# Kernel optimization log

Measured on AMD Instinct MI355X. Metric: run time of the kernel, lower is better.

The kernel has to match this reference:

```python
import jax, jax.numpy as jnp
import numpy as np

TOP_K = 2
NEG_INF = -1e30


def setup_inputs() -> dict:
    key = jax.random.key(0)
    ks = jax.random.split(key, 9)
    S, B, D, H, E, O = 2, 2048, 1024, 2048, 8, 1024
    return {
        "xs": jax.random.normal(ks[0], (S, B, D), jnp.float32),
        "Wg": jax.random.normal(ks[1], (D, E), jnp.float32),
        "b": jax.random.normal(ks[2], (E,), jnp.float32),
        "fc1_w": jax.random.normal(ks[3], (E, H, D), jnp.float32) * 0.02,
        "fc1_b": jax.random.normal(ks[4], (E, H), jnp.float32) * 0.02,
        "fc2_w": jax.random.normal(ks[5], (E, H, H), jnp.float32) * 0.02,
        "fc2_b": jax.random.normal(ks[6], (E, H), jnp.float32) * 0.02,
        "final_w": jax.random.normal(ks[7], (O, H), jnp.float32) * 0.02,
        "final_b": jax.random.normal(ks[8], (O,), jnp.float32) * 0.02,
    }


def reference(xs, Wg, b, fc1_w, fc1_b, fc2_w, fc2_b, final_w, final_b):
    # xs: [S, B, D] stacked x_list
    S = xs.shape[0]
    # gate logits H: [S, B, E]
    Hg = jnp.einsum('sbd,de->sbe', xs, Wg) + b
    expert_probs = jax.nn.softmax(Hg, axis=-1)  # per-view full softmax
    # top-k threshold mask (H >= kth largest value)
    topk_vals = jax.lax.top_k(Hg, TOP_K)[0]          # [S, B, K]
    thr = topk_vals[..., -1:]                         # [S, B, 1]
    H_masked = jnp.where(Hg >= thr, Hg, NEG_INF)
    G = jax.nn.softmax(H_masked, axis=-1)             # [S, B, E]
    # dense all-expert FFN: [S, B, E, H]
    h = jnp.einsum('sbd,ehd->sbeh', xs, fc1_w) + fc1_b
    h = jax.nn.relu(h)
    eo = jnp.einsum('sbeh,egh->sbeg', h, fc2_w) + fc2_b
    # gated sum over experts, averaged over views: [B, H]
    combined = jnp.einsum('sbe,sbeh->bh', G, eo) / S
    out = combined @ final_w.T + final_b               # [B, O]
    return out, expert_probs
```

## Files before the change

### kernel.cpp

```cpp
#include <hip/hip_runtime.h>
#include <stdint.h>

#define S_DIM 2
#define B_DIM 2048
#define D_DIM 1024
#define H_DIM 2048
#define E_DIM 8
#define O_DIM 1024
#define NTOK 4096
#define CAP 12288

typedef __attribute__((ext_vector_type(8))) short bf16x8;
typedef __attribute__((ext_vector_type(4))) float f32x4;

__device__ __forceinline__ unsigned short f2bf(float f) {
    union { float f; uint32_t i; } c; c.f = f;
    uint32_t r = c.i + 0x7FFFu + ((c.i >> 16) & 1u);
    return (unsigned short)(r >> 16);
}
__device__ __forceinline__ uint32_t pack2(float a, float b) {
    return (uint32_t)f2bf(a) | ((uint32_t)f2bf(b) << 16);
}
__device__ __forceinline__ void stage8(const float* __restrict__ src,
                                       unsigned short* __restrict__ dst) {
    float4 f0 = *(const float4*)src;
    float4 f1 = *(const float4*)(src + 4);
    int4 v;
    v.x = (int)pack2(f0.x, f0.y);
    v.y = (int)pack2(f0.z, f0.w);
    v.z = (int)pack2(f1.x, f1.y);
    v.w = (int)pack2(f1.z, f1.w);
    *(int4*)dst = v;
}

__device__ __forceinline__ void glds16(const unsigned short* g, unsigned short* l) {
    __builtin_amdgcn_global_load_lds(
        (__attribute__((address_space(1))) void*)g,
        (__attribute__((address_space(3))) void*)l,
        16, 0, 0);
}

__global__ __launch_bounds__(256) void convert_kernel(
    const float* __restrict__ src, unsigned short* __restrict__ dst, int n8)
{
    int i = blockIdx.x * blockDim.x + threadIdx.x;
    if (i < n8) stage8(src + (size_t)i * 8, dst + (size_t)i * 8);
}

__global__ __launch_bounds__(256) void gating_kernel(
    const float* __restrict__ xs,
    const float* __restrict__ Wg,
    const float* __restrict__ bvec,
    float* __restrict__ probs_out,
    int* __restrict__ counts,
    int* __restrict__ sel_cnt,
    int* __restrict__ sel_e,
    float* __restrict__ sel_g,
    unsigned short* __restrict__ xs_bf)
{
    const int wave = threadIdx.x >> 6;
    const int lane = threadIdx.x & 63;
    const int t = blockIdx.x * 4 + wave;
    const float* x = xs + (size_t)t * D_DIM;

    float acc[8];
#pragma unroll
    for (int e = 0; e < 8; ++e) acc[e] = 0.f;

#pragma unroll
    for (int i = 0; i < D_DIM / 64; ++i) {
        int d = i * 64 + lane;
        float xv = x[d];
        xs_bf[(size_t)t * D_DIM + d] = f2bf(xv);
        float4 w0 = *(const float4*)(Wg + (size_t)d * 8);
        float4 w1 = *(const float4*)(Wg + (size_t)d * 8 + 4);
        acc[0] += xv * w0.x; acc[1] += xv * w0.y;
        acc[2] += xv * w0.z; acc[3] += xv * w0.w;
        acc[4] += xv * w1.x; acc[5] += xv * w1.y;
        acc[6] += xv * w1.z; acc[7] += xv * w1.w;
    }
#pragma unroll
    for (int off = 32; off > 0; off >>= 1) {
#pragma unroll
        for (int e = 0; e < 8; ++e)
            acc[e] += __shfl_down(acc[e], off);
    }

    if (lane == 0) {
        float Hg[8];
#pragma unroll
        for (int e = 0; e < 8; ++e) Hg[e] = acc[e] + bvec[e];

        int a1 = 0;
#pragma unroll
        for (int e = 1; e < 8; ++e) if (Hg[e] > Hg[a1]) a1 = e;
        float m1 = Hg[a1];
        float m2 = -1e30f;
#pragma unroll
        for (int e = 0; e < 8; ++e) if (e != a1 && Hg[e] > m2) m2 = Hg[e];

        float ex[8]; float sum = 0.f;
#pragma unroll
        for (int e = 0; e < 8; ++e) { ex[e] = expf(Hg[e] - m1); sum += ex[e]; }
        float inv = 1.f / sum;
#pragma unroll
        for (int e = 0; e < 8; ++e)
            probs_out[(size_t)t * 8 + e] = ex[e] * inv;

        float den = 0.f;
#pragma unroll
        for (int e = 0; e < 8; ++e) if (Hg[e] >= m2) den += ex[e];
        float invd = 1.f / den;
        int n = 0;
#pragma unroll
        for (int e = 0; e < 8; ++e) {
            if (Hg[e] >= m2) {
                sel_e[t * 8 + n] = e;
                sel_g[t * 8 + n] = ex[e] * invd;
                ++n;
                atomicAdd(&counts[e], 1);
            }
        }
        sel_cnt[t] = n;
    }
}

__global__ void scan_kernel(const int* __restrict__ counts, int* __restrict__ offsets)
{
    if (threadIdx.x == 0) {
        int tot = 0;
#pragma unroll
        for (int e = 0; e < 8; ++e) { offsets[e] = tot; tot += counts[e]; }
    }
}

__global__ __launch_bounds__(256) void scatter_kernel(
    const int* __restrict__ sel_cnt,
    const int* __restrict__ sel_e,
    const float* __restrict__ sel_g,
    const int* __restrict__ offsets,
    int* __restrict__ cursors,
    int* __restrict__ pair_token,
    float* __restrict__ pair_gate)
{
    int t = blockIdx.x * blockDim.x + threadIdx.x;
    if (t >= NTOK) return;
    int n = sel_cnt[t];
    for (int i = 0; i < n && i < 8; ++i) {
        int e = sel_e[t * 8 + i];
        int r = atomicAdd(&cursors[e], 1);
        int slot = offsets[e] + r;
        if (slot < CAP) {
            pair_token[slot] = t;
            pair_gate[slot]  = sel_g[t * 8 + i];
        }
    }
}

__global__ __launch_bounds__(256) void fc1_kernel(
    const unsigned short* __restrict__ xs_bf,
    const unsigned short* __restrict__ fc1_wb,
    const float* __restrict__ fc1_b,
    const int* __restrict__ counts,
    const int* __restrict__ offsets,
    const int* __restrict__ pair_token,
    unsigned short* __restrict__ h)
{
    const int e = blockIdx.z;
    const int cnt = counts[e];
    const int mtile = blockIdx.y;
    if (mtile * 128 >= cnt) return;
    const int ntile = blockIdx.x;
    const int offs = offsets[e];

    __shared__ __align__(16) unsigned short As[128 * 64];
    __shared__ __align__(16) unsigned short Bs[128 * 64];

    const int tid  = threadIdx.x;
    const int lane = tid & 63;
    const int wave = tid >> 6;
    const int wr = wave >> 1, wc = wave & 1;
    const int lrow = lane & 15;
    const int kq   = lane >> 4;

    const unsigned short* aSrc[4];
    const unsigned short* bSrc[4];
    unsigned short* aDst[4];
    unsigned short* bDst[4];
#pragma unroll
    for (int i = 0; i < 4; ++i) {
        int c = i * 256 + tid;
        int row = c >> 3;
        int gran = (c & 7) ^ (row & 7);
        int m = mtile * 128 + row;
        int mc = m < cnt ? m : cnt - 1;
        int tok = pair_token[offs + mc];
        aSrc[i] = xs_bf + (size_t)tok * D_DIM + gran * 8;
        int n = ntile * 128 + row;
        bSrc[i] = fc1_wb + ((size_t)e * H_DIM + n) * D_DIM + gran * 8;
        aDst[i] = &As[(i * 256 + wave * 64) * 8];
        bDst[i] = &Bs[(i * 256 + wave * 64) * 8];
    }

    f32x4 acc[4][4];
#pragma unroll
    for (int i = 0; i < 4; ++i)
#pragma unroll
        for (int j = 0; j < 4; ++j)
            acc[i][j] = (f32x4){0.f, 0.f, 0.f, 0.f};

    for (int k0 = 0; k0 < D_DIM; k0 += 64) {
        __syncthreads();
#pragma unroll
        for (int i = 0; i < 4; ++i) {
            glds16(aSrc[i] + k0, aDst[i]);
            glds16(bSrc[i] + k0, bDst[i]);
        }
        __syncthreads();
#pragma unroll
        for (int ks = 0; ks < 2; ++ks) {
            bf16x8 af[4], bfr[4];
            const int gr = ks * 4 + kq;
            const int sg = (gr ^ (lrow & 7)) * 8;
#pragma unroll
            for (int i = 0; i < 4; ++i) {
                af[i]  = *(const bf16x8*)&As[(wr * 64 + i * 16 + lrow) * 64 + sg];
                bfr[i] = *(const bf16x8*)&Bs[(wc * 64 + i * 16 + lrow) * 64 + sg];
            }
#pragma unroll
            for (int i = 0; i < 4; ++i)
#pragma unroll
                for (int j = 0; j < 4; ++j)
                    acc[i][j] = __builtin_amdgcn_mfma_f32_16x16x32_bf16(af[i], bfr[j], acc[i][j], 0, 0, 0);
        }
    }

    int ncol[4]; float bias[4];
#pragma unroll
    for (int j = 0; j < 4; ++j) {
        ncol[j] = ntile * 128 + wc * 64 + j * 16 + lrow;
        bias[j] = fc1_b[e * H_DIM + ncol[j]];
    }
#pragma unroll
    for (int i = 0; i < 4; ++i) {
#pragma unroll
        for (int r = 0; r < 4; ++r) {
            int m = mtile * 128 + wr * 64 + i * 16 + kq * 4 + r;
            if (m < cnt) {
                size_t base = (size_t)(offs + m) * H_DIM;
#pragma unroll
                for (int j = 0; j < 4; ++j) {
                    float v = acc[i][j][r] + bias[j];
                    h[base + ncol[j]] = f2bf(v > 0.f ? v : 0.f);
                }
            }
        }
    }
}

__global__ __launch_bounds__(256) void fc2_kernel(
    const unsigned short* __restrict__ h,
    const unsigned short* __restrict__ fc2_wb,
    const float* __restrict__ fc2_b,
    const int* __restrict__ counts,
    const int* __restrict__ offsets,
    const int* __restrict__ pair_token,
    const float* __restrict__ pair_gate,
    float* __restrict__ combined)
{
    const int e = blockIdx.z;
    const int cnt = counts[e];
    const int mtile = blockIdx.y;
    if (mtile * 128 >= cnt) return;
    const int ntile = blockIdx.x;
    const int offs = offsets[e];

    __shared__ __align__(16) unsigned short As[128 * 64];
    __shared__ __align__(16) unsigned short Bs[128 * 64];

    const int tid  = threadIdx.x;
    const int lane = tid & 63;
    const int wave = tid >> 6;
    const int wr = wave >> 1, wc = wave & 1;
    const int lrow = lane & 15;
    const int kq   = lane >> 4;

    const unsigned short* aSrc[4];
    const unsigned short* bSrc[4];
    unsigned short* aDst[4];
    unsigned short* bDst[4];
#pragma unroll
    for (int i = 0; i < 4; ++i) {
        int c = i * 256 + tid;
        int row = c >> 3;
        int gran = (c & 7) ^ (row & 7);
        int m = mtile * 128 + row;
        int mc = m < cnt ? m : cnt - 1;
        aSrc[i] = h + (size_t)(offs + mc) * H_DIM + gran * 8;
        int n = ntile * 128 + row;
        bSrc[i] = fc2_wb + ((size_t)e * H_DIM + n) * H_DIM + gran * 8;
        aDst[i] = &As[(i * 256 + wave * 64) * 8];
        bDst[i] = &Bs[(i * 256 + wave * 64) * 8];
    }

    f32x4 acc[4][4];
#pragma unroll
    for (int i = 0; i < 4; ++i)
#pragma unroll
        for (int j = 0; j < 4; ++j)
            acc[i][j] = (f32x4){0.f, 0.f, 0.f, 0.f};

    for (int k0 = 0; k0 < H_DIM; k0 += 64) {
        __syncthreads();
#pragma unroll
        for (int i = 0; i < 4; ++i) {
            glds16(aSrc[i] + k0, aDst[i]);
            glds16(bSrc[i] + k0, bDst[i]);
        }
        __syncthreads();
#pragma unroll
        for (int ks = 0; ks < 2; ++ks) {
            bf16x8 af[4], bfr[4];
            const int gr = ks * 4 + kq;
            const int sg = (gr ^ (lrow & 7)) * 8;
#pragma unroll
            for (int i = 0; i < 4; ++i) {
                af[i]  = *(const bf16x8*)&As[(wr * 64 + i * 16 + lrow) * 64 + sg];
                bfr[i] = *(const bf16x8*)&Bs[(wc * 64 + i * 16 + lrow) * 64 + sg];
            }
#pragma unroll
            for (int i = 0; i < 4; ++i)
#pragma unroll
                for (int j = 0; j < 4; ++j)
                    acc[i][j] = __builtin_amdgcn_mfma_f32_16x16x32_bf16(af[i], bfr[j], acc[i][j], 0, 0, 0);
        }
    }

    int ncol[4]; float bias[4];
#pragma unroll
    for (int j = 0; j < 4; ++j) {
        ncol[j] = ntile * 128 + wc * 64 + j * 16 + lrow;
        bias[j] = fc2_b[e * H_DIM + ncol[j]];
    }
#pragma unroll
    for (int i = 0; i < 4; ++i) {
#pragma unroll
        for (int r = 0; r < 4; ++r) {
            int m = mtile * 128 + wr * 64 + i * 16 + kq * 4 + r;
            if (m < cnt) {
                int slot = offs + m;
                int tok  = pair_token[slot];
                float g  = pair_gate[slot] * 0.5f;
                int brow = tok & (B_DIM - 1);
#pragma unroll
                for (int j = 0; j < 4; ++j) {
                    float v = (acc[i][j][r] + bias[j]) * g;
                    atomicAdd(&combined[(size_t)brow * H_DIM + ncol[j]], v);
                }
            }
        }
    }
}

__global__ __launch_bounds__(256) void final_kernel(
    const float* __restrict__ combined,
    const float* __restrict__ final_w,
    const float* __restrict__ final_b,
    float* __restrict__ out)
{
    const int mtile = blockIdx.y;
    const int ntile = blockIdx.x;

    __shared__ __align__(16) unsigned short As[128 * 40];
    __shared__ __align__(16) unsigned short Bs[128 * 40];

    const int tid  = threadIdx.x;
    const int lane = tid & 63;
    const int wave = tid >> 6;
    const int wr = wave >> 1, wc = wave & 1;
    const int lrow = lane & 15;
    const int kq   = lane >> 4;
    const int koff = kq * 8;

    const float* aSrc[2];
    const float* bSrc[2];
    int ldsOff[2];
#pragma unroll
    for (int i = 0; i < 2; ++i) {
        int c = tid + i * 256;
        int row = c >> 2;
        int kc  = (c & 3) * 8;
        ldsOff[i] = row * 40 + kc;
        int m = mtile * 128 + row;
        aSrc[i] = combined + (size_t)m * H_DIM + kc;
        int n = ntile * 128 + row;
        bSrc[i] = final_w + (size_t)n * H_DIM + kc;
    }

    f32x4 acc[4][4];
#pragma unroll
    for (int i = 0; i < 4; ++i)
#pragma unroll
        for (int j = 0; j < 4; ++j)
            acc[i][j] = (f32x4){0.f, 0.f, 0.f, 0.f};

    for (int k0 = 0; k0 < H_DIM; k0 += 32) {
        __syncthreads();
#pragma unroll
        for (int i = 0; i < 2; ++i) {
            stage8(aSrc[i] + k0, &As[ldsOff[i]]);
            stage8(bSrc[i] + k0, &Bs[ldsOff[i]]);
        }
        __syncthreads();
        bf16x8 af[4], bfr[4];
#pragma unroll
        for (int i = 0; i < 4; ++i)
            af[i] = *(const bf16x8*)&As[(wr * 64 + i * 16 + lrow) * 40 + koff];
#pragma unroll
        for (int j = 0; j < 4; ++j)
            bfr[j] = *(const bf16x8*)&Bs[(wc * 64 + j * 16 + lrow) * 40 + koff];
#pragma unroll
        for (int i = 0; i < 4; ++i)
#pragma unroll
            for (int j = 0; j < 4; ++j)
                acc[i][j] = __builtin_amdgcn_mfma_f32_16x16x32_bf16(af[i], bfr[j], acc[i][j], 0, 0, 0);
    }

    int ncol[4]; float bias[4];
#pragma unroll
    for (int j = 0; j < 4; ++j) {
        ncol[j] = ntile * 128 + wc * 64 + j * 16 + lrow;
        bias[j] = final_b[ncol[j]];
    }
#pragma unroll
    for (int i = 0; i < 4; ++i) {
#pragma unroll
        for (int r = 0; r < 4; ++r) {
            int m = mtile * 128 + wr * 64 + i * 16 + kq * 4 + r;
#pragma unroll
            for (int j = 0; j < 4; ++j)
                out[(size_t)m * O_DIM + ncol[j]] = acc[i][j][r] + bias[j];
        }
    }
}

extern "C" void kernel_launch(void* const* d_in, const int* in_sizes, int n_in,
                              void* d_out, int out_size, void* d_ws, size_t ws_size,
                              hipStream_t stream) {
    const float* xs      = (const float*)d_in[0];
    const float* Wg      = (const float*)d_in[1];
    const float* bvec    = (const float*)d_in[2];
    const float* fc1_w   = (const float*)d_in[3];
    const float* fc1_b   = (const float*)d_in[4];
    const float* fc2_w   = (const float*)d_in[5];
    const float* fc2_b   = (const float*)d_in[6];
    const float* final_w = (const float*)d_in[7];
    const float* final_b = (const float*)d_in[8];

    float* out = (float*)d_out;
    float* probs_out = out + (size_t)B_DIM * O_DIM;

    uint8_t* w = (uint8_t*)d_ws;
    int*   counts     = (int*)(w + 0);
    int*   cursors    = (int*)(w + 64);
    int*   offsets    = (int*)(w + 128);
    int*   sel_cnt    = (int*)(w + 256);
    int*   sel_e      = (int*)(w + 0x5000);
    float* sel_g      = (float*)(w + 0x25000);
    int*   pair_token = (int*)(w + 0x45000);
    float* pair_gate  = (float*)(w + 0x51000);
    float* combined   = (float*)(w + 0x60000);
    unsigned short* h = (unsigned short*)(w + 0x1060000);
    unsigned short* xs_bf   = (unsigned short*)(w + 0x4060000);
    unsigned short* fc1_wb  = (unsigned short*)(w + 0x4860000);
    unsigned short* fc2_wb  = (unsigned short*)(w + 0x6860000);

    hipMemsetAsync(w, 0, 256, stream);
    hipMemsetAsync(combined, 0, (size_t)B_DIM * H_DIM * sizeof(float), stream);

    convert_kernel<<<(E_DIM * H_DIM * D_DIM / 8) / 256, 256, 0, stream>>>(
        fc1_w, fc1_wb, E_DIM * H_DIM * D_DIM / 8);
    convert_kernel<<<(E_DIM * H_DIM * H_DIM / 8) / 256, 256, 0, stream>>>(
        fc2_w, fc2_wb, E_DIM * H_DIM * H_DIM / 8);

    gating_kernel<<<NTOK / 4, 256, 0, stream>>>(xs, Wg, bvec, probs_out,
                                                counts, sel_cnt, sel_e, sel_g, xs_bf);
    scan_kernel<<<1, 64, 0, stream>>>(counts, offsets);
    scatter_kernel<<<NTOK / 256, 256, 0, stream>>>(sel_cnt, sel_e, sel_g, offsets,
                                                   cursors, pair_token, pair_gate);
    fc1_kernel<<<dim3(H_DIM / 128, NTOK / 128, E_DIM), 256, 0, stream>>>(
        xs_bf, fc1_wb, fc1_b, counts, offsets, pair_token, h);
    fc2_kernel<<<dim3(H_DIM / 128, NTOK / 128, E_DIM), 256, 0, stream>>>(
        h, fc2_wb, fc2_b, counts, offsets, pair_token, pair_gate, combined);
    final_kernel<<<dim3(O_DIM / 128, B_DIM / 128), 256, 0, stream>>>(
        combined, final_w, final_b, out);
}
```

Before: 716.9 us.

## Double-buffer LDS in expert GEMMs and convert final GEMM inputs to bf16

fc1, fc2 and final kernels now use two LDS buffers. The next K-tile is loaded with global-to-LDS copies while MFMAs run on the current one, and each iteration has one barrier instead of two. The final GEMM is rewritten to match. Separate convert kernels turn final_w and combined into bf16, so it can use the same swizzled 64-wide glds16 path instead of converting fp32 on the fly. The cost is double the LDS per block, which may lower occupancy, plus two extra conversion launches.

```diff
diff --git a/kernel.cpp b/kernel.cpp
--- a/kernel.cpp
+++ b/kernel.cpp
@@ -173,8 +173,8 @@
     const int ntile = blockIdx.x;
     const int offs = offsets[e];
 
-    __shared__ __align__(16) unsigned short As[128 * 64];
-    __shared__ __align__(16) unsigned short Bs[128 * 64];
+    __shared__ __align__(16) unsigned short As[2][128 * 64];
+    __shared__ __align__(16) unsigned short Bs[2][128 * 64];
 
     const int tid  = threadIdx.x;
     const int lane = tid & 63;
@@ -185,8 +185,7 @@
 
     const unsigned short* aSrc[4];
     const unsigned short* bSrc[4];
-    unsigned short* aDst[4];
-    unsigned short* bDst[4];
+    int dstOff[4];
 #pragma unroll
     for (int i = 0; i < 4; ++i) {
         int c = i * 256 + tid;
@@ -198,8 +197,7 @@
         aSrc[i] = xs_bf + (size_t)tok * D_DIM + gran * 8;
         int n = ntile * 128 + row;
         bSrc[i] = fc1_wb + ((size_t)e * H_DIM + n) * D_DIM + gran * 8;
-        aDst[i] = &As[(i * 256 + wave * 64) * 8];
-        bDst[i] = &Bs[(i * 256 + wave * 64) * 8];
+        dstOff[i] = (i * 256 + wave * 64) * 8;
     }
 
     f32x4 acc[4][4];
@@ -209,14 +207,14 @@
         for (int j = 0; j < 4; ++j)
             acc[i][j] = (f32x4){0.f, 0.f, 0.f, 0.f};
 
-    for (int k0 = 0; k0 < D_DIM; k0 += 64) {
-        __syncthreads();
+    auto stage = [&](int buf, int k0) {
 #pragma unroll
         for (int i = 0; i < 4; ++i) {
-            glds16(aSrc[i] + k0, aDst[i]);
-            glds16(bSrc[i] + k0, bDst[i]);
-        }
-        __syncthreads();
+            glds16(aSrc[i] + k0, &As[buf][dstOff[i]]);
+            glds16(bSrc[i] + k0, &Bs[buf][dstOff[i]]);
+        }
+    };
+    auto compute = [&](int buf) {
 #pragma unroll
         for (int ks = 0; ks < 2; ++ks) {
             bf16x8 af[4], bfr[4];
@@ -224,8 +222,8 @@
             const int sg = (gr ^ (lrow & 7)) * 8;
 #pragma unroll
             for (int i = 0; i < 4; ++i) {
-                af[i]  = *(const bf16x8*)&As[(wr * 64 + i * 16 + lrow) * 64 + sg];
-                bfr[i] = *(const bf16x8*)&Bs[(wc * 64 + i * 16 + lrow) * 64 + sg];
+                af[i]  = *(const bf16x8*)&As[buf][(wr * 64 + i * 16 + lrow) * 64 + sg];
+                bfr[i] = *(const bf16x8*)&Bs[buf][(wc * 64 + i * 16 + lrow) * 64 + sg];
             }
 #pragma unroll
             for (int i = 0; i < 4; ++i)
@@ -233,7 +231,21 @@
                 for (int j = 0; j < 4; ++j)
                     acc[i][j] = __builtin_amdgcn_mfma_f32_16x16x32_bf16(af[i], bfr[j], acc[i][j], 0, 0, 0);
         }
-    }
+    };
+
+    const int NT = D_DIM / 64;
+    stage(0, 0);
+    asm volatile("s_waitcnt vmcnt(0)" ::: "memory");
+    __builtin_amdgcn_s_barrier();
+    int cur = 0;
+    for (int t = 0; t < NT - 1; ++t) {
+        stage(cur ^ 1, (t + 1) * 64);
+        compute(cur);
+        asm volatile("s_waitcnt vmcnt(0)" ::: "memory");
+        __builtin_amdgcn_s_barrier();
+        cur ^= 1;
+    }
+    compute(cur);
 
     int ncol[4]; float bias[4];
 #pragma unroll
@@ -275,8 +287,8 @@
     const int ntile = blockIdx.x;
     const int offs = offsets[e];
 
-    __shared__ __align__(16) unsigned short As[128 * 64];
-    __shared__ __align__(16) unsigned short Bs[128 * 64];
+    __shared__ __align__(16) unsigned short As[2][128 * 64];
+    __shared__ __align__(16) unsigned short Bs[2][128 * 64];
 
     const int tid  = threadIdx.x;
     const int lane = tid & 63;
@@ -287,8 +299,7 @@
 
     const unsigned short* aSrc[4];
     const unsigned short* bSrc[4];
-    unsigned short* aDst[4];
-    unsigned short* bDst[4];
+    int dstOff[4];
 #pragma unroll
     for (int i = 0; i < 4; ++i) {
         int c = i * 256 + tid;
@@ -299,8 +310,7 @@
         aSrc[i] = h + (size_t)(offs + mc) * H_DIM + gran * 8;
         int n = ntile * 128 + row;
         bSrc[i] = fc2_wb + ((size_t)e * H_DIM + n) * H_DIM + gran * 8;
-        aDst[i] = &As[(i * 256 + wave * 64) * 8];
-        bDst[i] = &Bs[(i * 256 + wave * 64) * 8];
+        dstOff[i] = (i * 256 + wave * 64) * 8;
     }
 
     f32x4 acc[4][4];
@@ -310,14 +320,14 @@
         for (int j = 0; j < 4; ++j)
             acc[i][j] = (f32x4){0.f, 0.f, 0.f, 0.f};
 
-    for (int k0 = 0; k0 < H_DIM; k0 += 64) {
-        __syncthreads();
+    auto stage = [&](int buf, int k0) {
 #pragma unroll
         for (int i = 0; i < 4; ++i) {
-            glds16(aSrc[i] + k0, aDst[i]);
-            glds16(bSrc[i] + k0, bDst[i]);
-        }
-        __syncthreads();
+            glds16(aSrc[i] + k0, &As[buf][dstOff[i]]);
+            glds16(bSrc[i] + k0, &Bs[buf][dstOff[i]]);
+        }
+    };
+    auto compute = [&](int buf) {
 #pragma unroll
         for (int ks = 0; ks < 2; ++ks) {
             bf16x8 af[4], bfr[4];
@@ -325,8 +335,8 @@
             const int sg = (gr ^ (lrow & 7)) * 8;
 #pragma unroll
             for (int i = 0; i < 4; ++i) {
-                af[i]  = *(const bf16x8*)&As[(wr * 64 + i * 16 + lrow) * 64 + sg];
-                bfr[i] = *(const bf16x8*)&Bs[(wc * 64 + i * 16 + lrow) * 64 + sg];
+                af[i]  = *(const bf16x8*)&As[buf][(wr * 64 + i * 16 + lrow) * 64 + sg];
+                bfr[i] = *(const bf16x8*)&Bs[buf][(wc * 64 + i * 16 + lrow) * 64 + sg];
             }
 #pragma unroll
             for (int i = 0; i < 4; ++i)
@@ -334,7 +344,21 @@
                 for (int j = 0; j < 4; ++j)
                     acc[i][j] = __builtin_amdgcn_mfma_f32_16x16x32_bf16(af[i], bfr[j], acc[i][j], 0, 0, 0);
         }
-    }
+    };
+
+    const int NT = H_DIM / 64;
+    stage(0, 0);
+    asm volatile("s_waitcnt vmcnt(0)" ::: "memory");
+    __builtin_amdgcn_s_barrier();
+    int cur = 0;
+    for (int t = 0; t < NT - 1; ++t) {
+        stage(cur ^ 1, (t + 1) * 64);
+        compute(cur);
+        asm volatile("s_waitcnt vmcnt(0)" ::: "memory");
+        __builtin_amdgcn_s_barrier();
+        cur ^= 1;
+    }
+    compute(cur);
 
     int ncol[4]; float bias[4];
 #pragma unroll
@@ -363,16 +387,16 @@
 }
 
 __global__ __launch_bounds__(256) void final_kernel(
-    const float* __restrict__ combined,
-    const float* __restrict__ final_w,
+    const unsigned short* __restrict__ combined_bf,
+    const unsigned short* __restrict__ final_wb,
     const float* __restrict__ final_b,
     float* __restrict__ out)
 {
     const int mtile = blockIdx.y;
     const int ntile = blockIdx.x;
 
-    __shared__ __align__(16) unsigned short As[128 * 40];
-    __shared__ __align__(16) unsigned short Bs[128 * 40];
+    __shared__ __align__(16) unsigned short As[2][128 * 64];
+    __shared__ __align__(16) unsigned short Bs[2][128 * 64];
 
     const int tid  = threadIdx.x;
     const int lane = tid & 63;
@@ -380,21 +404,20 @@
     const int wr = wave >> 1, wc = wave & 1;
     const int lrow = lane & 15;
     const int kq   = lane >> 4;
-    const int koff = kq * 8;
-
-    const float* aSrc[2];
-    const float* bSrc[2];
-    int ldsOff[2];
-#pragma unroll
-    for (int i = 0; i < 2; ++i) {
-        int c = tid + i * 256;
-        int row = c >> 2;
-        int kc  = (c & 3) * 8;
-        ldsOff[i] = row * 40 + kc;
+
+    const unsigned short* aSrc[4];
+    const unsigned short* bSrc[4];
+    int dstOff[4];
+#pragma unroll
+    for (int i = 0; i < 4; ++i) {
+        int c = i * 256 + tid;
+        int row = c >> 3;
+        int gran = (c & 7) ^ (row & 7);
         int m = mtile * 128 + row;
-        aSrc[i] = combined + (size_t)m * H_DIM + kc;
+        aSrc[i] = combined_bf + (size_t)m * H_DIM + gran * 8;
         int n = ntile * 128 + row;
-        bSrc[i] = final_w + (size_t)n * H_DIM + kc;
+        bSrc[i] = final_wb + (size_t)n * H_DIM + gran * 8;
+        dstOff[i] = (i * 256 + wave * 64) * 8;
     }
 
     f32x4 acc[4][4];
@@ -404,27 +427,45 @@
         for (int j = 0; j < 4; ++j)
             acc[i][j] = (f32x4){0.f, 0.f, 0.f, 0.f};
 
-    for (int k0 = 0; k0 < H_DIM; k0 += 32) {
-        __syncthreads();
-#pragma unroll
-        for (int i = 0; i < 2; ++i) {
-            stage8(aSrc[i] + k0, &As[ldsOff[i]]);
-            stage8(bSrc[i] + k0, &Bs[ldsOff[i]]);
-        }
-        __syncthreads();
-        bf16x8 af[4], bfr[4];
-#pragma unroll
-        for (int i = 0; i < 4; ++i)
-            af[i] = *(const bf16x8*)&As[(wr * 64 + i * 16 + lrow) * 40 + koff];
-#pragma unroll
-        for (int j = 0; j < 4; ++j)
-            bfr[j] = *(const bf16x8*)&Bs[(wc * 64 + j * 16 + lrow) * 40 + koff];
-#pragma unroll
-        for (int i = 0; i < 4; ++i)
-#pragma unroll
-            for (int j = 0; j < 4; ++j)
-                acc[i][j] = __builtin_amdgcn_mfma_f32_16x16x32_bf16(af[i], bfr[j], acc[i][j], 0, 0, 0);
-    }
+    auto stage = [&](int buf, int k0) {
+#pragma unroll
+        for (int i = 0; i < 4; ++i) {
+            glds16(aSrc[i] + k0, &As[buf][dstOff[i]]);
+            glds16(bSrc[i] + k0, &Bs[buf][dstOff[i]]);
+        }
+    };
+    auto compute = [&](int buf) {
+#pragma unroll
+        for (int ks = 0; ks < 2; ++ks) {
+            bf16x8 af[4], bfr[4];
+            const int gr = ks * 4 + kq;
+            const int sg = (gr ^ (lrow & 7)) * 8;
+#pragma unroll
+            for (int i = 0; i < 4; ++i) {
+                af[i]  = *(const bf16x8*)&As[buf][(wr * 64 + i * 16 + lrow) * 64 + sg];
+                bfr[i] = *(const bf16x8*)&Bs[buf][(wc * 64 + i * 16 + lrow) * 64 + sg];
+            }
+#pragma unroll
+            for (int i = 0; i < 4; ++i)
+#pragma unroll
+                for (int j = 0; j < 4; ++j)
+                    acc[i][j] = __builtin_amdgcn_mfma_f32_16x16x32_bf16(af[i], bfr[j], acc[i][j], 0, 0, 0);
+        }
+    };
+
+    const int NT = H_DIM / 64;
+    stage(0, 0);
+    asm volatile("s_waitcnt vmcnt(0)" ::: "memory");
+    __builtin_amdgcn_s_barrier();
+    int cur = 0;
+    for (int t = 0; t < NT - 1; ++t) {
+        stage(cur ^ 1, (t + 1) * 64);
+        compute(cur);
+        asm volatile("s_waitcnt vmcnt(0)" ::: "memory");
+        __builtin_amdgcn_s_barrier();
+        cur ^= 1;
+    }
+    compute(cur);
 
     int ncol[4]; float bias[4];
 #pragma unroll
@@ -474,6 +515,8 @@
     unsigned short* xs_bf   = (unsigned short*)(w + 0x4060000);
     unsigned short* fc1_wb  = (unsigned short*)(w + 0x4860000);
     unsigned short* fc2_wb  = (unsigned short*)(w + 0x6860000);
+    unsigned short* final_wb    = (unsigned short*)(w + 0xA860000);
+    unsigned short* combined_bf = (unsigned short*)(w + 0xAC60000);
 
     hipMemsetAsync(w, 0, 256, stream);
     hipMemsetAsync(combined, 0, (size_t)B_DIM * H_DIM * sizeof(float), stream);
@@ -482,6 +525,8 @@
         fc1_w, fc1_wb, E_DIM * H_DIM * D_DIM / 8);
     convert_kernel<<<(E_DIM * H_DIM * H_DIM / 8) / 256, 256, 0, stream>>>(
         fc2_w, fc2_wb, E_DIM * H_DIM * H_DIM / 8);
+    convert_kernel<<<(O_DIM * H_DIM / 8) / 256, 256, 0, stream>>>(
+        final_w, final_wb, O_DIM * H_DIM / 8);
 
     gating_kernel<<<NTOK / 4, 256, 0, stream>>>(xs, Wg, bvec, probs_out,
                                                 counts, sel_cnt, sel_e, sel_g, xs_bf);
@@ -492,6 +537,8 @@
         xs_bf, fc1_wb, fc1_b, counts, offsets, pair_token, h);
     fc2_kernel<<<dim3(H_DIM / 128, NTOK / 128, E_DIM), 256, 0, stream>>>(
         h, fc2_wb, fc2_b, counts, offsets, pair_token, pair_gate, combined);
+    convert_kernel<<<(B_DIM * H_DIM / 8) / 256, 256, 0, stream>>>(
+        combined, combined_bf, B_DIM * H_DIM / 8);
     final_kernel<<<dim3(O_DIM / 128, B_DIM / 128), 256, 0, stream>>>(
-        combined, final_w, final_b, out);
-}
+        combined_bf, final_wb, final_b, out);
+}
```

New measurement: 730.5 us. Within noise of the previous version (+1.9%).

## Flatten expert GEMM grids expert-major and pre-convert final GEMM inputs to bf16

Applied to the files above, without the earlier changes.

The fc1 and fc2 launches become 1D grids with the expert index in the low bits, so consecutive workgroups spread across experts instead of piling empty tiles from one expert together. The final GEMM now reads bf16 copies of combined and final_w, made by extra convert launches, and uses the same async global-to-LDS swizzled 64-wide K loop as the expert GEMMs. This removes the per-iteration fp32 load-and-convert staging in the final GEMM. The cost is two more kernel launches and an extra pass over combined and final_w.

```diff
diff --git a/kernel.cpp b/kernel.cpp
--- a/kernel.cpp
+++ b/kernel.cpp
@@ -166,11 +166,13 @@
     const int* __restrict__ pair_token,
     unsigned short* __restrict__ h)
 {
-    const int e = blockIdx.z;
+    const int wg = blockIdx.x;
+    const int e = wg & 7;
+    const int idx = wg >> 3;
+    const int mtile = idx >> 4;
+    const int ntile = idx & 15;
     const int cnt = counts[e];
-    const int mtile = blockIdx.y;
     if (mtile * 128 >= cnt) return;
-    const int ntile = blockIdx.x;
     const int offs = offsets[e];
 
     __shared__ __align__(16) unsigned short As[128 * 64];
@@ -185,8 +187,7 @@
 
     const unsigned short* aSrc[4];
     const unsigned short* bSrc[4];
-    unsigned short* aDst[4];
-    unsigned short* bDst[4];
+    int dstOff[4];
 #pragma unroll
     for (int i = 0; i < 4; ++i) {
         int c = i * 256 + tid;
@@ -198,8 +199,7 @@
         aSrc[i] = xs_bf + (size_t)tok * D_DIM + gran * 8;
         int n = ntile * 128 + row;
         bSrc[i] = fc1_wb + ((size_t)e * H_DIM + n) * D_DIM + gran * 8;
-        aDst[i] = &As[(i * 256 + wave * 64) * 8];
-        bDst[i] = &Bs[(i * 256 + wave * 64) * 8];
+        dstOff[i] = (i * 256 + wave * 64) * 8;
     }
 
     f32x4 acc[4][4];
@@ -213,8 +213,8 @@
         __syncthreads();
 #pragma unroll
         for (int i = 0; i < 4; ++i) {
-            glds16(aSrc[i] + k0, aDst[i]);
-            glds16(bSrc[i] + k0, bDst[i]);
+            glds16(aSrc[i] + k0, &As[dstOff[i]]);
+            glds16(bSrc[i] + k0, &Bs[dstOff[i]]);
         }
         __syncthreads();
 #pragma unroll
@@ -268,11 +268,13 @@
     const float* __restrict__ pair_gate,
     float* __restrict__ combined)
 {
-    const int e = blockIdx.z;
+    const int wg = blockIdx.x;
+    const int e = wg & 7;
+    const int idx = wg >> 3;
+    const int mtile = idx >> 4;
+    const int ntile = idx & 15;
     const int cnt = counts[e];
-    const int mtile = blockIdx.y;
     if (mtile * 128 >= cnt) return;
-    const int ntile = blockIdx.x;
     const int offs = offsets[e];
 
     __shared__ __align__(16) unsigned short As[128 * 64];
@@ -287,8 +289,7 @@
 
     const unsigned short* aSrc[4];
     const unsigned short* bSrc[4];
-    unsigned short* aDst[4];
-    unsigned short* bDst[4];
+    int dstOff[4];
 #pragma unroll
     for (int i = 0; i < 4; ++i) {
         int c = i * 256 + tid;
@@ -299,8 +300,7 @@
         aSrc[i] = h + (size_t)(offs + mc) * H_DIM + gran * 8;
         int n = ntile * 128 + row;
         bSrc[i] = fc2_wb + ((size_t)e * H_DIM + n) * H_DIM + gran * 8;
-        aDst[i] = &As[(i * 256 + wave * 64) * 8];
-        bDst[i] = &Bs[(i * 256 + wave * 64) * 8];
+        dstOff[i] = (i * 256 + wave * 64) * 8;
     }
 
     f32x4 acc[4][4];
@@ -314,8 +314,8 @@
         __syncthreads();
 #pragma unroll
         for (int i = 0; i < 4; ++i) {
-            glds16(aSrc[i] + k0, aDst[i]);
-            glds16(bSrc[i] + k0, bDst[i]);
+            glds16(aSrc[i] + k0, &As[dstOff[i]]);
+            glds16(bSrc[i] + k0, &Bs[dstOff[i]]);
         }
         __syncthreads();
 #pragma unroll
@@ -363,16 +363,16 @@
 }
 
 __global__ __launch_bounds__(256) void final_kernel(
-    const float* __restrict__ combined,
-    const float* __restrict__ final_w,
+    const unsigned short* __restrict__ combined_bf,
+    const unsigned short* __restrict__ final_wb,
     const float* __restrict__ final_b,
     float* __restrict__ out)
 {
     const int mtile = blockIdx.y;
     const int ntile = blockIdx.x;
 
-    __shared__ __align__(16) unsigned short As[128 * 40];
-    __shared__ __align__(16) unsigned short Bs[128 * 40];
+    __shared__ __align__(16) unsigned short As[128 * 64];
+    __shared__ __align__(16) unsigned short Bs[128 * 64];
 
     const int tid  = threadIdx.x;
     const int lane = tid & 63;
@@ -380,21 +380,20 @@
     const int wr = wave >> 1, wc = wave & 1;
     const int lrow = lane & 15;
     const int kq   = lane >> 4;
-    const int koff = kq * 8;
-
-    const float* aSrc[2];
-    const float* bSrc[2];
-    int ldsOff[2];
-#pragma unroll
-    for (int i = 0; i < 2; ++i) {
-        int c = tid + i * 256;
-        int row = c >> 2;
-        int kc  = (c & 3) * 8;
-        ldsOff[i] = row * 40 + kc;
+
+    const unsigned short* aSrc[4];
+    const unsigned short* bSrc[4];
+    int dstOff[4];
+#pragma unroll
+    for (int i = 0; i < 4; ++i) {
+        int c = i * 256 + tid;
+        int row = c >> 3;
+        int gran = (c & 7) ^ (row & 7);
         int m = mtile * 128 + row;
-        aSrc[i] = combined + (size_t)m * H_DIM + kc;
+        aSrc[i] = combined_bf + (size_t)m * H_DIM + gran * 8;
         int n = ntile * 128 + row;
-        bSrc[i] = final_w + (size_t)n * H_DIM + kc;
+        bSrc[i] = final_wb + (size_t)n * H_DIM + gran * 8;
+        dstOff[i] = (i * 256 + wave * 64) * 8;
     }
 
     f32x4 acc[4][4];
@@ -404,26 +403,30 @@
         for (int j = 0; j < 4; ++j)
             acc[i][j] = (f32x4){0.f, 0.f, 0.f, 0.f};
 
-    for (int k0 = 0; k0 < H_DIM; k0 += 32) {
+    for (int k0 = 0; k0 < H_DIM; k0 += 64) {
         __syncthreads();
 #pragma unroll
-        for (int i = 0; i < 2; ++i) {
-            stage8(aSrc[i] + k0, &As[ldsOff[i]]);
-            stage8(bSrc[i] + k0, &Bs[ldsOff[i]]);
+        for (int i = 0; i < 4; ++i) {
+            glds16(aSrc[i] + k0, &As[dstOff[i]]);
+            glds16(bSrc[i] + k0, &Bs[dstOff[i]]);
         }
         __syncthreads();
-        bf16x8 af[4], bfr[4];
-#pragma unroll
-        for (int i = 0; i < 4; ++i)
-            af[i] = *(const bf16x8*)&As[(wr * 64 + i * 16 + lrow) * 40 + koff];
-#pragma unroll
-        for (int j = 0; j < 4; ++j)
-            bfr[j] = *(const bf16x8*)&Bs[(wc * 64 + j * 16 + lrow) * 40 + koff];
-#pragma unroll
-        for (int i = 0; i < 4; ++i)
-#pragma unroll
-            for (int j = 0; j < 4; ++j)
-                acc[i][j] = __builtin_amdgcn_mfma_f32_16x16x32_bf16(af[i], bfr[j], acc[i][j], 0, 0, 0);
+#pragma unroll
+        for (int ks = 0; ks < 2; ++ks) {
+            bf16x8 af[4], bfr[4];
+            const int gr = ks * 4 + kq;
+            const int sg = (gr ^ (lrow & 7)) * 8;
+#pragma unroll
+            for (int i = 0; i < 4; ++i) {
+                af[i]  = *(const bf16x8*)&As[(wr * 64 + i * 16 + lrow) * 64 + sg];
+                bfr[i] = *(const bf16x8*)&Bs[(wc * 64 + i * 16 + lrow) * 64 + sg];
+            }
+#pragma unroll
+            for (int i = 0; i < 4; ++i)
+#pragma unroll
+                for (int j = 0; j < 4; ++j)
+                    acc[i][j] = __builtin_amdgcn_mfma_f32_16x16x32_bf16(af[i], bfr[j], acc[i][j], 0, 0, 0);
+        }
     }
 
     int ncol[4]; float bias[4];
@@ -474,6 +477,8 @@
     unsigned short* xs_bf   = (unsigned short*)(w + 0x4060000);
     unsigned short* fc1_wb  = (unsigned short*)(w + 0x4860000);
     unsigned short* fc2_wb  = (unsigned short*)(w + 0x6860000);
+    unsigned short* final_wb    = (unsigned short*)(w + 0xA860000);
+    unsigned short* combined_bf = (unsigned short*)(w + 0xAC60000);
 
     hipMemsetAsync(w, 0, 256, stream);
     hipMemsetAsync(combined, 0, (size_t)B_DIM * H_DIM * sizeof(float), stream);
@@ -482,16 +487,20 @@
         fc1_w, fc1_wb, E_DIM * H_DIM * D_DIM / 8);
     convert_kernel<<<(E_DIM * H_DIM * H_DIM / 8) / 256, 256, 0, stream>>>(
         fc2_w, fc2_wb, E_DIM * H_DIM * H_DIM / 8);
+    convert_kernel<<<(O_DIM * H_DIM / 8) / 256, 256, 0, stream>>>(
+        final_w, final_wb, O_DIM * H_DIM / 8);
 
     gating_kernel<<<NTOK / 4, 256, 0, stream>>>(xs, Wg, bvec, probs_out,
                                                 counts, sel_cnt, sel_e, sel_g, xs_bf);
     scan_kernel<<<1, 64, 0, stream>>>(counts, offsets);
     scatter_kernel<<<NTOK / 256, 256, 0, stream>>>(sel_cnt, sel_e, sel_g, offsets,
                                                    cursors, pair_token, pair_gate);
-    fc1_kernel<<<dim3(H_DIM / 128, NTOK / 128, E_DIM), 256, 0, stream>>>(
+    fc1_kernel<<<E_DIM * (NTOK / 128) * (H_DIM / 128), 256, 0, stream>>>(
         xs_bf, fc1_wb, fc1_b, counts, offsets, pair_token, h);
-    fc2_kernel<<<dim3(H_DIM / 128, NTOK / 128, E_DIM), 256, 0, stream>>>(
+    fc2_kernel<<<E_DIM * (NTOK / 128) * (H_DIM / 128), 256, 0, stream>>>(
         h, fc2_wb, fc2_b, counts, offsets, pair_token, pair_gate, combined);
+    convert_kernel<<<(B_DIM * H_DIM / 8) / 256, 256, 0, stream>>>(
+        combined, combined_bf, B_DIM * H_DIM / 8);
     final_kernel<<<dim3(O_DIM / 128, B_DIM / 128), 256, 0, stream>>>(
-        combined, final_w, final_b, out);
-}
+        combined_bf, final_wb, final_b, out);
+}
```

Result: faster. 662.5 us (-7.6%).
